# Performance work log

Measured on AMD Instinct MI355X. Metric: run time of the kernel, lower is better.

## Reference

```python
import jax, jax.numpy as jnp
import numpy as np

BS, C_OUT, D = 8192, 50000, 64
CLAMP_MIN, CLAMP_MAX = 1e-12, 1e12


def setup_inputs() -> dict:
    key = jax.random.key(0)
    k1, k2, k3 = jax.random.split(key, 3)
    x = jax.random.normal(k1, (BS, D), dtype=jnp.float32)
    labels = jax.random.randint(k2, (BS,), 0, C_OUT, dtype=jnp.int64)
    centers = jax.random.normal(k3, (C_OUT, D), dtype=jnp.float32)
    return {"x": x, "labels": labels, "centers": centers}


def reference(x, labels, centers):
    bs, c_out = x.shape[0], centers.shape[0]
    # full pairwise squared-distance matrix [bs, c_out] (faithful to torch addmm path)
    distmat = (
        jnp.sum(x * x, axis=1, keepdims=True)            # [bs, 1]
        + jnp.sum(centers * centers, axis=1)[None, :]     # [1, c_out]
        - 2.0 * (x @ centers.T)                           # [bs, c_out]
    )
    mask = (labels[:, None] == jnp.arange(c_out)[None, :]).astype(distmat.dtype)
    dist = distmat * mask
    # NOTE: the original clamps AFTER masking, so the bs*(c_out-1) zeroed entries
    # each contribute 1e-12 to the sum; we reproduce that exactly.
    loss = jnp.clip(dist, CLAMP_MIN, CLAMP_MAX).sum() / bs
    return loss
```

## Files before the change

### kernel.cpp

```cpp
#include <hip/hip_runtime.h>


#define BS_N 8192
#define C_OUT_N 50000
#define D_N 64

#define NBLOCKS 2048
#define NTHREADS 256

__global__ void center_loss_partial(const float* __restrict__ x,
                                    const int* __restrict__ labels,
                                    const float* __restrict__ centers,
                                    float* __restrict__ partials) {
    const int gtid   = blockIdx.x * blockDim.x + threadIdx.x;
    const int wave   = gtid >> 6;
    const int lane   = threadIdx.x & 63;
    const int nwaves = (gridDim.x * blockDim.x) >> 6;

    float acc = 0.0f;
    for (int row = wave; row < BS_N; row += nwaves) {
        const int lbl = labels[row];
        const float xv = x[row * D_N + lane];
        const float cv = centers[lbl * D_N + lane];
        const float d  = xv - cv;
        float v = d * d;
        #pragma unroll
        for (int off = 32; off > 0; off >>= 1)
            v += __shfl_down(v, off, 64);
        if (lane == 0) {
            v = fminf(fmaxf(v, 1e-12f), 1e12f);
            acc += v;
        }
    }

    __shared__ float smem[NTHREADS / 64];
    const int wib = threadIdx.x >> 6;
    if (lane == 0) smem[wib] = acc;
    __syncthreads();
    if (threadIdx.x == 0) {
        float s = 0.0f;
        #pragma unroll
        for (int i = 0; i < NTHREADS / 64; ++i) s += smem[i];
        partials[blockIdx.x] = s;
    }
}

__global__ void center_loss_final(const float* __restrict__ partials,
                                  float* __restrict__ out) {
    float v = 0.0f;
    for (int i = threadIdx.x; i < NBLOCKS; i += blockDim.x) v += partials[i];
    #pragma unroll
    for (int off = 32; off > 0; off >>= 1)
        v += __shfl_down(v, off, 64);

    __shared__ float smem[NTHREADS / 64];
    const int lane = threadIdx.x & 63;
    const int wib  = threadIdx.x >> 6;
    if (lane == 0) smem[wib] = v;
    __syncthreads();
    if (threadIdx.x == 0) {
        float s = 0.0f;
        #pragma unroll
        for (int i = 0; i < NTHREADS / 64; ++i) s += smem[i];
        double loss = (double)s / (double)BS_N
                    + (double)(C_OUT_N - 1) * 1e-12;
        out[0] = (float)loss;
    }
}

extern "C" void kernel_launch(void* const* d_in, const int* in_sizes, int n_in,
                              void* d_out, int out_size, void* d_ws, size_t ws_size,
                              hipStream_t stream) {
    const float* x       = (const float*)d_in[0];
    const int*   labels  = (const int*)d_in[1];
    const float* centers = (const float*)d_in[2];
    float*       out     = (float*)d_out;
    float*       partials = (float*)d_ws;

    center_loss_partial<<<NBLOCKS, NTHREADS, 0, stream>>>(x, labels, centers, partials);
    center_loss_final<<<1, NTHREADS, 0, stream>>>(partials, out);
}
```

Measured before the change: 13.26 us.

## Fuse partial and final reduction into one cooperative kernel with float4 loads

Replaces the two-kernel reduction with a single cooperative launch that uses a grid-wide sync before block 0 sums the per-block partials, removing the second kernel launch. Each row is now handled by 16 lanes loading float4s instead of a full wave of scalar loads, and the grid shrinks from 2048 to 256 blocks. Cooperative launch and grid sync add their own overhead, and fewer blocks may expose less memory-level parallelism for the gathered center rows.

```diff
diff --git a/kernel.cpp b/kernel.cpp
--- a/kernel.cpp
+++ b/kernel.cpp
@@ -1,82 +1,90 @@
 #include <hip/hip_runtime.h>
+#include <hip/hip_cooperative_groups.h>
+
+namespace cg = cooperative_groups;
 
 
 #define BS_N 8192
 #define C_OUT_N 50000
 #define D_N 64
 
-#define NBLOCKS 2048
+#define NBLOCKS 256
 #define NTHREADS 256
 
-__global__ void center_loss_partial(const float* __restrict__ x,
-                                    const int* __restrict__ labels,
-                                    const float* __restrict__ centers,
-                                    float* __restrict__ partials) {
-    const int gtid   = blockIdx.x * blockDim.x + threadIdx.x;
-    const int wave   = gtid >> 6;
-    const int lane   = threadIdx.x & 63;
-    const int nwaves = (gridDim.x * blockDim.x) >> 6;
+__global__ void center_loss_fused(const float* __restrict__ x,
+                                  const int* __restrict__ labels,
+                                  const float* __restrict__ centers,
+                                  float* __restrict__ partials,
+                                  float* __restrict__ out) {
+    const int tid  = threadIdx.x;
+    const int gtid = blockIdx.x * NTHREADS + tid;
+    const int sub  = tid & 15;
+    const int row_stride = (NBLOCKS * NTHREADS) / 16;
 
     float acc = 0.0f;
-    for (int row = wave; row < BS_N; row += nwaves) {
+    for (int row = gtid >> 4; row < BS_N; row += row_stride) {
         const int lbl = labels[row];
-        const float xv = x[row * D_N + lane];
-        const float cv = centers[lbl * D_N + lane];
-        const float d  = xv - cv;
-        float v = d * d;
+        const float4 xv = *(const float4*)(x + row * D_N + sub * 4);
+        const float4 cv = *(const float4*)(centers + lbl * D_N + sub * 4);
+        const float dx = xv.x - cv.x;
+        const float dy = xv.y - cv.y;
+        const float dz = xv.z - cv.z;
+        const float dw = xv.w - cv.w;
+        float v = dx * dx + dy * dy + dz * dz + dw * dw;
+        v += __shfl_xor(v, 8, 64);
+        v += __shfl_xor(v, 4, 64);
+        v += __shfl_xor(v, 2, 64);
+        v += __shfl_xor(v, 1, 64);
+        if (sub == 0) acc += fminf(fmaxf(v, 1e-12f), 1e12f);
+    }
+
+    #pragma unroll
+    for (int off = 32; off > 0; off >>= 1)
+        acc += __shfl_down(acc, off, 64);
+
+    __shared__ float smem[NTHREADS / 64];
+    if ((tid & 63) == 0) smem[tid >> 6] = acc;
+    __syncthreads();
+    if (tid == 0) {
+        const float s = smem[0] + smem[1] + smem[2] + smem[3];
+        __hip_atomic_store(&partials[blockIdx.x], s,
+                           __ATOMIC_RELEASE, __HIP_MEMORY_SCOPE_AGENT);
+    }
+
+    cg::this_grid().sync();
+
+    if (blockIdx.x == 0) {
+        float v = (tid < NBLOCKS)
+                ? __hip_atomic_load(&partials[tid],
+                                    __ATOMIC_ACQUIRE, __HIP_MEMORY_SCOPE_AGENT)
+                : 0.0f;
         #pragma unroll
         for (int off = 32; off > 0; off >>= 1)
             v += __shfl_down(v, off, 64);
-        if (lane == 0) {
-            v = fminf(fmaxf(v, 1e-12f), 1e12f);
-            acc += v;
+        __shared__ float smem2[NTHREADS / 64];
+        if ((tid & 63) == 0) smem2[tid >> 6] = v;
+        __syncthreads();
+        if (tid == 0) {
+            const float s = smem2[0] + smem2[1] + smem2[2] + smem2[3];
+            const double loss = (double)s / (double)BS_N
+                              + (double)(C_OUT_N - 1) * 1e-12;
+            out[0] = (float)loss;
         }
-    }
-
-    __shared__ float smem[NTHREADS / 64];
-    const int wib = threadIdx.x >> 6;
-    if (lane == 0) smem[wib] = acc;
-    __syncthreads();
-    if (threadIdx.x == 0) {
-        float s = 0.0f;
-        #pragma unroll
-        for (int i = 0; i < NTHREADS / 64; ++i) s += smem[i];
-        partials[blockIdx.x] = s;
-    }
-}
-
-__global__ void center_loss_final(const float* __restrict__ partials,
-                                  float* __restrict__ out) {
-    float v = 0.0f;
-    for (int i = threadIdx.x; i < NBLOCKS; i += blockDim.x) v += partials[i];
-    #pragma unroll
-    for (int off = 32; off > 0; off >>= 1)
-        v += __shfl_down(v, off, 64);
-
-    __shared__ float smem[NTHREADS / 64];
-    const int lane = threadIdx.x & 63;
-    const int wib  = threadIdx.x >> 6;
-    if (lane == 0) smem[wib] = v;
-    __syncthreads();
-    if (threadIdx.x == 0) {
-        float s = 0.0f;
-        #pragma unroll
-        for (int i = 0; i < NTHREADS / 64; ++i) s += smem[i];
-        double loss = (double)s / (double)BS_N
-                    + (double)(C_OUT_N - 1) * 1e-12;
-        out[0] = (float)loss;
     }
 }
 
 extern "C" void kernel_launch(void* const* d_in, const int* in_sizes, int n_in,
                               void* d_out, int out_size, void* d_ws, size_t ws_size,
                               hipStream_t stream) {
-    const float* x       = (const float*)d_in[0];
-    const int*   labels  = (const int*)d_in[1];
-    const float* centers = (const float*)d_in[2];
-    float*       out     = (float*)d_out;
+    const float* x        = (const float*)d_in[0];
+    const int*   labels   = (const int*)d_in[1];
+    const float* centers  = (const float*)d_in[2];
+    float*       out      = (float*)d_out;
     float*       partials = (float*)d_ws;
 
-    center_loss_partial<<<NBLOCKS, NTHREADS, 0, stream>>>(x, labels, centers, partials);
-    center_loss_final<<<1, NTHREADS, 0, stream>>>(partials, out);
+    void* args[] = {(void*)&x, (void*)&labels, (void*)&centers,
+                    (void*)&partials, (void*)&out};
+    hipLaunchCooperativeKernel((void*)center_loss_fused,
+                               dim3(NBLOCKS), dim3(NTHREADS),
+                               args, 0, stream);
 }
```

Result: slower. 43.52 us (+228.2%).
